# Kernel optimization log

Hardware: AMD Instinct MI355X
Metric: run time of the kernel (lower is better)

The kernel has to match this reference:

```python
import jax, jax.numpy as jnp
import numpy as np

B, S, HID = 8, 1024, 1024
NH, HD = 16, 64  # num heads, head dim
EPS = 1e-12


def setup_inputs() -> dict:
    key = jax.random.key(0)
    ks = jax.random.split(key, 8)
    sc = 0.02
    return {
        "hidden_states": jax.random.normal(ks[0], (B, S, HID), jnp.float32),
        "attention_mask": jnp.zeros((B, 1, 1, S), jnp.bool_),
        "rel_pos": jax.random.normal(ks[1], (1, NH, S, S), jnp.float32),
        "rel_2d_pos": jax.random.normal(ks[2], (1, NH, S, S), jnp.float32),
        "w_qkv": jax.random.normal(ks[3], (3 * HID, HID), jnp.float32) * sc,
        "q_bias": jnp.zeros((1, 1, HID), jnp.float32),
        "v_bias": jnp.zeros((1, 1, HID), jnp.float32),
        "w_out": jax.random.normal(ks[4], (HID, HID), jnp.float32) * sc,
        "b_out": jnp.zeros((HID,), jnp.float32),
        "ln_gamma": jnp.ones((HID,), jnp.float32),
        "ln_beta": jnp.zeros((HID,), jnp.float32),
    }


def reference(hidden_states, attention_mask, rel_pos, rel_2d_pos,
              w_qkv, q_bias, v_bias, w_out, b_out, ln_gamma, ln_beta):
    x = hidden_states
    # fast_qkv: single projection, no bias; then add q_bias/v_bias
    qkv = jnp.einsum('bsh,oh->bso', x, w_qkv)  # [B,S,3*HID]
    q, k, v = jnp.split(qkv, 3, axis=-1)
    q = q + q_bias
    v = v + v_bias
    # [B,S,HID] -> [B,NH,S,HD]
    to_heads = lambda t: t.reshape(B, S, NH, HD).transpose(0, 2, 1, 3)
    qh, kh, vh = to_heads(q), to_heads(k), to_heads(v)
    qh = qh / jnp.sqrt(jnp.float32(HD))
    scores = jnp.einsum('bhqd,bhkd->bhqk', qh, kh)
    scores = scores + rel_pos + rel_2d_pos
    scores = jnp.where(attention_mask, -jnp.inf, scores.astype(jnp.float32))
    probs = jax.nn.softmax(scores, axis=-1).astype(vh.dtype)
    ctx = jnp.einsum('bhqk,bhkd->bhqd', probs, vh)
    ctx = ctx.transpose(0, 2, 1, 3).reshape(B, S, HID)
    # self-output: dense + residual + LayerNorm
    h = jnp.einsum('bsh,oh->bso', ctx, w_out) + b_out + x
    mu = jnp.mean(h, axis=-1, keepdims=True)
    var = jnp.var(h, axis=-1, keepdims=True)
    out = (h - mu) / jnp.sqrt(var + EPS) * ln_gamma + ln_beta
    return out
```

## Files before the change

kernel.cpp:

```cpp
#include <hip/hip_runtime.h>
#include <stdint.h>
#include <stddef.h>

typedef unsigned short u16;
typedef __attribute__((ext_vector_type(8))) short short8;
typedef __attribute__((ext_vector_type(4))) float f32x4;
typedef __attribute__((ext_vector_type(4))) unsigned short ushort4v;
typedef __attribute__((ext_vector_type(4))) unsigned char uchar4v;
typedef __attribute__((ext_vector_type(2))) unsigned int uint2v;

constexpr int B_ = 8, S_ = 1024, HID_ = 1024, NH_ = 16, HD_ = 64;

__device__ __forceinline__ u16 f2b(float f) {
  unsigned int u = __builtin_bit_cast(unsigned int, f);
  u += 0x7fff + ((u >> 16) & 1);
  return (u16)(u >> 16);
}
__device__ __forceinline__ float b2f(u16 s) {
  unsigned int u = ((unsigned int)s) << 16;
  return __builtin_bit_cast(float, u);
}
__device__ __forceinline__ void llds16(const void* g, void* l) {
  __builtin_amdgcn_global_load_lds((__attribute__((address_space(1))) void*)g,
                                   (__attribute__((address_space(3))) void*)l, 16, 0, 0);
}

__global__ __launch_bounds__(256) void prep_cvt(
    const float* __restrict__ x, const float* __restrict__ wqkv,
    const float* __restrict__ wout, u16* __restrict__ xb,
    u16* __restrict__ wqkvb, u16* __restrict__ woutb) {
  const int NX4 = B_ * S_ * HID_ / 4, NW14 = 3 * HID_ * HID_ / 4, NW24 = HID_ * HID_ / 4;
  const int tot = NX4 + NW14 + NW24;
  for (int i = blockIdx.x * blockDim.x + threadIdx.x; i < tot; i += gridDim.x * blockDim.x) {
    const float4* s; u16* d; int j;
    if (i < NX4)              { s = (const float4*)x;    d = xb;    j = i; }
    else if (i < NX4 + NW14)  { s = (const float4*)wqkv; d = wqkvb; j = i - NX4; }
    else                      { s = (const float4*)wout; d = woutb; j = i - NX4 - NW14; }
    float4 v = s[j];
    ushort4v o; o[0] = f2b(v.x); o[1] = f2b(v.y); o[2] = f2b(v.z); o[3] = f2b(v.w);
    *(ushort4v*)(d + 4 * (size_t)j) = o;
  }
}

__global__ __launch_bounds__(256) void rel_perm(
    const float* __restrict__ a, const float* __restrict__ b, u16* __restrict__ relb) {
  __shared__ u16 lbuf[16 * 1032];
  const int qtg = blockIdx.x, h = blockIdx.y;
  const int t = threadIdx.x;
#pragma unroll
  for (int it = 0; it < 16; ++it) {
    int idx = it * 256 + t;
    int lq = idx >> 8, kc = idx & 255;
    size_t src = ((size_t)h * S_ + qtg * 16 + lq) * S_ + kc * 4;
    float4 va = *(const float4*)(a + src);
    float4 vb = *(const float4*)(b + src);
    ushort4v o;
    o[0] = f2b(va.x + vb.x); o[1] = f2b(va.y + vb.y);
    o[2] = f2b(va.z + vb.z); o[3] = f2b(va.w + vb.w);
    *(ushort4v*)(lbuf + lq * 1032 + kc * 4) = o;
  }
  __syncthreads();
#pragma unroll
  for (int it = 0; it < 16; ++it) {
    int c = it * 16 + (t >> 4);
    int ktg = c >> 2, qk = c & 3, lq = t & 15;
    ushort4v v = *(const ushort4v*)(lbuf + lq * 1032 + ktg * 16 + qk * 4);
    *(ushort4v*)(relb + ((((size_t)h * 64 + ktg) * 64 + qtg) * 4 + qk) * 64 + lq * 4) = v;
  }
}

__global__ __launch_bounds__(256) void gemm_qkv(
    const u16* __restrict__ W, const u16* __restrict__ X,
    const float* __restrict__ qbias, const float* __restrict__ vbias,
    u16* __restrict__ Qb, u16* __restrict__ Kb, u16* __restrict__ Vb) {
  constexpr int K = HID_;
  __shared__ u16 smem[128 * 136];
  u16* Ws = smem;
  u16* Xs = smem + 4096;
  const int o0 = blockIdx.x * 128, s0 = blockIdx.y * 128;
  const int t = threadIdx.x, lane = t & 63, wv = t >> 6;
  const int wr = wv >> 1, wc = wv & 1, ln = lane & 15, q8 = lane >> 4;
  f32x4 acc[4][4] = {};

  for (int kt = 0; kt < K / 32; ++kt) {
    const int k0 = kt * 32;
#pragma unroll
    for (int c = 0; c < 2; ++c) {
      int idx = c * 256 + t, row = idx >> 2, cc = (idx & 3) * 8;
      llds16(W + (size_t)(o0 + row) * K + k0 + cc, Ws + (size_t)(c * 256 + wv * 64) * 8);
      llds16(X + (size_t)(s0 + row) * K + k0 + cc, Xs + (size_t)(c * 256 + wv * 64) * 8);
    }
    __syncthreads();
    short8 of[4], sf[4];
#pragma unroll
    for (int mi = 0; mi < 4; ++mi)
      of[mi] = *(const short8*)(Ws + (wr * 64 + mi * 16 + ln) * 32 + q8 * 8);
#pragma unroll
    for (int ni = 0; ni < 4; ++ni)
      sf[ni] = *(const short8*)(Xs + (wc * 64 + ni * 16 + ln) * 32 + q8 * 8);
#pragma unroll
    for (int mi = 0; mi < 4; ++mi)
#pragma unroll
      for (int ni = 0; ni < 4; ++ni)
        acc[mi][ni] = __builtin_amdgcn_mfma_f32_16x16x32_bf16(of[mi], sf[ni], acc[mi][ni], 0, 0, 0);
    __syncthreads();
  }

  const int sec = o0 >> 10;
#pragma unroll
  for (int mi = 0; mi < 4; ++mi) {
    const int ocol = wr * 64 + mi * 16 + q8 * 4;
    const int oo = (o0 + ocol) & 1023;
    float4 b4;
    if (sec == 0)      b4 = *(const float4*)(qbias + oo);
    else if (sec == 2) b4 = *(const float4*)(vbias + oo);
    else               b4 = float4{0.f, 0.f, 0.f, 0.f};
#pragma unroll
    for (int ni = 0; ni < 4; ++ni) {
      const int srow = wc * 64 + ni * 16 + ln;
      u16 e[4];
#pragma unroll
      for (int r = 0; r < 4; ++r) {
        float v = acc[mi][ni][r] + ((const float*)&b4)[r];
        if (sec == 0) v *= 0.125f;
        e[r] = f2b(v);
      }
      uint2v pw;
      pw[0] = (unsigned)e[0] | ((unsigned)e[1] << 16);
      pw[1] = (unsigned)e[2] | ((unsigned)e[3] << 16);
      *(uint2v*)(smem + srow * 136 + ocol) = pw;
    }
  }
  __syncthreads();
  u16* dst = (sec == 0) ? Qb : (sec == 1) ? Kb : Vb;
#pragma unroll
  for (int i = 0; i < 8; ++i) {
    int flat = i * 256 + t;
    int srow = flat >> 4, c8 = (flat & 15) * 8;
    short8 v = *(const short8*)(smem + srow * 136 + c8);
    int oo = (o0 + c8) & 1023, hh = oo >> 6, dd = oo & 63;
    int s = s0 + srow, bb = s >> 10, ss = s & 1023;
    *(short8*)(dst + ((size_t)(bb * NH_ + hh) * S_ + ss) * HD_ + dd) = v;
  }
}

__global__ __launch_bounds__(256) void transpose_v(
    const u16* __restrict__ Vb, u16* __restrict__ Vtb) {
  __shared__ u16 tile[64][72];
  const int st = blockIdx.x * 64, bh = blockIdx.y;
  const int t = threadIdx.x;
#pragma unroll
  for (int i = 0; i < 2; ++i) {
    int idx = i * 256 + t, row = idx >> 3, c8 = (idx & 7) * 8;
    *(short8*)(&tile[row][c8]) = *(const short8*)(Vb + ((size_t)bh * S_ + st + row) * HD_ + c8);
  }
  __syncthreads();
#pragma unroll
  for (int i = 0; i < 2; ++i) {
    int idx = i * 256 + t, d = idx >> 3, c8 = (idx & 7) * 8;
    short8 v;
#pragma unroll
    for (int j = 0; j < 8; ++j) v[j] = (short)tile[c8 + j][d];
    *(short8*)(Vtb + ((size_t)bh * HD_ + d) * S_ + st + c8) = v;
  }
}

__global__ __launch_bounds__(256, 3) void flash_attn(
    const u16* __restrict__ Qb, const u16* __restrict__ Kb,
    const u16* __restrict__ Vtb, const u16* __restrict__ relb,
    const unsigned char* __restrict__ mask, u16* __restrict__ ctxb) {
  const int qt_blk = blockIdx.x, h = blockIdx.y, b = blockIdx.z;
  const int bh = b * NH_ + h, q0 = qt_blk * 128;
  const int t = threadIdx.x, lane = t & 63, wv = t >> 6;
  const int ln = lane & 15, q8 = lane >> 4;

  __shared__ u16 Ks[128 * 72];
  __shared__ u16 Vts[64 * 136];
  __shared__ u16 Pbuf[4 * 32 * 40];
  u16* Pw = Pbuf + wv * 1280;

  const int krow = t >> 3, kcol = (t & 7) * 8;
  const int vrow = t >> 4, vcol = (t & 15) * 8;

  short8 kreg[4], vreg[4];
#pragma unroll
  for (int i = 0; i < 4; ++i)
    kreg[i] = *(const short8*)(Kb + ((size_t)bh * S_ + i * 32 + krow) * HD_ + kcol);
#pragma unroll
  for (int i = 0; i < 4; ++i)
    vreg[i] = *(const short8*)(Vtb + ((size_t)bh * HD_ + i * 16 + vrow) * S_ + vcol);

  short8 qf[2][2];
#pragma unroll
  for (int qt = 0; qt < 2; ++qt)
#pragma unroll
    for (int kc = 0; kc < 2; ++kc)
      qf[qt][kc] = *(const short8*)(Qb + ((size_t)bh * S_ + q0 + wv * 32 + qt * 16 + ln) * HD_ + kc * 32 + q8 * 8);

  f32x4 Oa[4][2] = {};
  float rs2[2] = {0.f, 0.f};

  for (int kt128 = 0; kt128 < 8; ++kt128) {
    const int k0 = kt128 * 128;

    ushort4v relg[4][2][2];
    uchar4v  mg[4][2];
#pragma unroll
    for (int kvc = 0; kvc < 4; ++kvc)
#pragma unroll
      for (int sub = 0; sub < 2; ++sub) {
        const int kt = kvc * 2 + sub, ktg = kt128 * 8 + kt;
        mg[kvc][sub] = *(const uchar4v*)(mask + b * S_ + k0 + kt * 16 + q8 * 4);
#pragma unroll
        for (int qt = 0; qt < 2; ++qt) {
          const int qtg = qt_blk * 8 + wv * 2 + qt;
          relg[kvc][sub][qt] = *(const ushort4v*)(relb +
              ((((size_t)h * 64 + ktg) * 64 + qtg) * 4 + q8) * 64 + ln * 4);
        }
      }

    __syncthreads();
#pragma unroll
    for (int i = 0; i < 4; ++i)
      *(short8*)(Ks + (i * 32 + krow) * 72 + kcol) = kreg[i];
#pragma unroll
    for (int i = 0; i < 4; ++i)
      *(short8*)(Vts + (i * 16 + vrow) * 136 + vcol) = vreg[i];
    if (kt128 < 7) {
      const int k0n = k0 + 128;
#pragma unroll
      for (int i = 0; i < 4; ++i)
        kreg[i] = *(const short8*)(Kb + ((size_t)bh * S_ + k0n + i * 32 + krow) * HD_ + kcol);
#pragma unroll
      for (int i = 0; i < 4; ++i)
        vreg[i] = *(const short8*)(Vtb + ((size_t)bh * HD_ + i * 16 + vrow) * S_ + k0n + vcol);
    }
    __syncthreads();

#pragma unroll
    for (int kvc = 0; kvc < 4; ++kvc) {
#pragma unroll
      for (int sub = 0; sub < 2; ++sub) {
        const int kt = kvc * 2 + sub;
        short8 kf0 = *(const short8*)(Ks + (kt * 16 + ln) * 72 + q8 * 8);
        short8 kf1 = *(const short8*)(Ks + (kt * 16 + ln) * 72 + 32 + q8 * 8);
        uchar4v m4 = mg[kvc][sub];
        f32x4 mbase;
#pragma unroll
        for (int r = 0; r < 4; ++r) mbase[r] = (m4[r] ? -1e30f : 0.f) - 8.0f;
#pragma unroll
        for (int qt = 0; qt < 2; ++qt) {
          ushort4v r4 = relg[kvc][sub][qt];
          f32x4 sc;
#pragma unroll
          for (int r = 0; r < 4; ++r) sc[r] = b2f(r4[r]) + mbase[r];
          sc = __builtin_amdgcn_mfma_f32_16x16x32_bf16(kf0, qf[qt][0], sc, 0, 0, 0);
          sc = __builtin_amdgcn_mfma_f32_16x16x32_bf16(kf1, qf[qt][1], sc, 0, 0, 0);
          float p0 = __expf(sc[0]), p1 = __expf(sc[1]);
          float p2 = __expf(sc[2]), p3 = __expf(sc[3]);
          rs2[qt] += (p0 + p1) + (p2 + p3);
          uint2v pw;
          pw[0] = (unsigned)f2b(p0) | ((unsigned)f2b(p1) << 16);
          pw[1] = (unsigned)f2b(p2) | ((unsigned)f2b(p3) << 16);
          *(uint2v*)(Pw + (qt * 16 + ln) * 40 + sub * 16 + q8 * 4) = pw;
        }
      }
      short8 pf0 = *(const short8*)(Pw + ln * 40 + q8 * 8);
      short8 pf1 = *(const short8*)(Pw + (16 + ln) * 40 + q8 * 8);
#pragma unroll
      for (int mt = 0; mt < 4; ++mt) {
        short8 vf = *(const short8*)(Vts + (mt * 16 + ln) * 136 + kvc * 32 + q8 * 8);
        Oa[mt][0] = __builtin_amdgcn_mfma_f32_16x16x32_bf16(vf, pf0, Oa[mt][0], 0, 0, 0);
        Oa[mt][1] = __builtin_amdgcn_mfma_f32_16x16x32_bf16(vf, pf1, Oa[mt][1], 0, 0, 0);
      }
    }
  }

  float inv[2];
#pragma unroll
  for (int qt = 0; qt < 2; ++qt) {
    rs2[qt] += __shfl_xor(rs2[qt], 16, 64);
    rs2[qt] += __shfl_xor(rs2[qt], 32, 64);
    inv[qt] = 1.f / rs2[qt];
  }

  __syncthreads();
  u16* Ob = Ks + wv * 2304;
#pragma unroll
  for (int qt = 0; qt < 2; ++qt)
#pragma unroll
    for (int mt = 0; mt < 4; ++mt) {
      u16 e[4];
#pragma unroll
      for (int r = 0; r < 4; ++r) e[r] = f2b(Oa[mt][qt][r] * inv[qt]);
      uint2v pw;
      pw[0] = (unsigned)e[0] | ((unsigned)e[1] << 16);
      pw[1] = (unsigned)e[2] | ((unsigned)e[3] << 16);
      *(uint2v*)(Ob + (qt * 16 + ln) * 72 + mt * 16 + q8 * 4) = pw;
    }
#pragma unroll
  for (int p = 0; p < 4; ++p) {
    int row = p * 8 + (lane >> 3);
    int c8 = (lane & 7) * 8;
    short8 v = *(const short8*)(Ob + row * 72 + c8);
    int q = q0 + wv * 32 + row;
    *(short8*)(ctxb + ((size_t)(b * S_ + q)) * HID_ + h * 64 + c8) = v;
  }
}

__global__ __launch_bounds__(256) void gemm_out(
    const u16* __restrict__ W, const u16* __restrict__ X,
    const float* __restrict__ bout, const float* __restrict__ xres,
    u16* __restrict__ hb) {
  constexpr int K = HID_;
  __shared__ u16 smem[128 * 136];
  u16* Ws = smem;
  u16* Xs = smem + 4096;
  const int o0 = blockIdx.x * 128, s0 = blockIdx.y * 128;
  const int t = threadIdx.x, lane = t & 63, wv = t >> 6;
  const int wr = wv >> 1, wc = wv & 1, ln = lane & 15, q8 = lane >> 4;
  f32x4 acc[4][4] = {};

  for (int kt = 0; kt < K / 32; ++kt) {
    const int k0 = kt * 32;
#pragma unroll
    for (int c = 0; c < 2; ++c) {
      int idx = c * 256 + t, row = idx >> 2, cc = (idx & 3) * 8;
      llds16(W + (size_t)(o0 + row) * K + k0 + cc, Ws + (size_t)(c * 256 + wv * 64) * 8);
      llds16(X + (size_t)(s0 + row) * K + k0 + cc, Xs + (size_t)(c * 256 + wv * 64) * 8);
    }
    __syncthreads();
    short8 of[4], sf[4];
#pragma unroll
    for (int mi = 0; mi < 4; ++mi)
      of[mi] = *(const short8*)(Ws + (wr * 64 + mi * 16 + ln) * 32 + q8 * 8);
#pragma unroll
    for (int ni = 0; ni < 4; ++ni)
      sf[ni] = *(const short8*)(Xs + (wc * 64 + ni * 16 + ln) * 32 + q8 * 8);
#pragma unroll
    for (int mi = 0; mi < 4; ++mi)
#pragma unroll
      for (int ni = 0; ni < 4; ++ni)
        acc[mi][ni] = __builtin_amdgcn_mfma_f32_16x16x32_bf16(of[mi], sf[ni], acc[mi][ni], 0, 0, 0);
    __syncthreads();
  }

#pragma unroll
  for (int mi = 0; mi < 4; ++mi) {
    const int ocol = wr * 64 + mi * 16 + q8 * 4;
    float4 b4 = *(const float4*)(bout + o0 + ocol);
#pragma unroll
    for (int ni = 0; ni < 4; ++ni) {
      const int srow = wc * 64 + ni * 16 + ln;
      u16 e[4];
#pragma unroll
      for (int r = 0; r < 4; ++r) e[r] = f2b(acc[mi][ni][r] + ((const float*)&b4)[r]);
      uint2v pw;
      pw[0] = (unsigned)e[0] | ((unsigned)e[1] << 16);
      pw[1] = (unsigned)e[2] | ((unsigned)e[3] << 16);
      *(uint2v*)(smem + srow * 136 + ocol) = pw;
    }
  }
  __syncthreads();
#pragma unroll
  for (int i = 0; i < 8; ++i) {
    int flat = i * 256 + t;
    int srow = flat >> 4, c8 = (flat & 15) * 8;
    short8 v = *(const short8*)(smem + srow * 136 + c8);
    int s = s0 + srow, o = o0 + c8;
    float4 x0 = *(const float4*)(xres + (size_t)s * HID_ + o);
    float4 x1 = *(const float4*)(xres + (size_t)s * HID_ + o + 4);
    short8 st;
#pragma unroll
    for (int j = 0; j < 4; ++j) st[j] = (short)f2b(b2f((u16)v[j]) + ((const float*)&x0)[j]);
#pragma unroll
    for (int j = 0; j < 4; ++j) st[4 + j] = (short)f2b(b2f((u16)v[4 + j]) + ((const float*)&x1)[j]);
    *(short8*)(hb + (size_t)s * HID_ + o) = st;
  }
}

__global__ __launch_bounds__(256) void ln_kernel(
    const u16* __restrict__ hb, const float* __restrict__ gamma,
    const float* __restrict__ beta, float* __restrict__ out) {
  const int lane = threadIdx.x & 63, wv = threadIdx.x >> 6;
  const int row = blockIdx.x * 4 + wv;
  const u16* hr = hb + (size_t)row * HID_;
  float v[16];
  short8 a = *(const short8*)(hr + lane * 16);
  short8 c = *(const short8*)(hr + lane * 16 + 8);
#pragma unroll
  for (int j = 0; j < 8; ++j) { v[j] = b2f((u16)a[j]); v[8 + j] = b2f((u16)c[j]); }
  float sum = 0.f, sq = 0.f;
#pragma unroll
  for (int j = 0; j < 16; ++j) { sum += v[j]; sq += v[j] * v[j]; }
#pragma unroll
  for (int off = 1; off < 64; off <<= 1) {
    sum += __shfl_xor(sum, off, 64);
    sq  += __shfl_xor(sq, off, 64);
  }
  const float mu = sum * (1.f / HID_);
  const float var = sq * (1.f / HID_) - mu * mu;
  const float inv = 1.f / sqrtf(var + 1e-12f);
#pragma unroll
  for (int j = 0; j < 16; ++j) {
    const int n = lane * 16 + j;
    out[(size_t)row * HID_ + n] = (v[j] - mu) * inv * gamma[n] + beta[n];
  }
}

extern "C" void kernel_launch(void* const* d_in, const int* in_sizes, int n_in,
                              void* d_out, int out_size, void* d_ws, size_t ws_size,
                              hipStream_t stream) {
  (void)in_sizes; (void)n_in; (void)out_size; (void)ws_size;
  const float* x     = (const float*)d_in[0];
  const unsigned char* mask = (const unsigned char*)d_in[1];
  const float* relp  = (const float*)d_in[2];
  const float* rel2  = (const float*)d_in[3];
  const float* wqkv  = (const float*)d_in[4];
  const float* qbias = (const float*)d_in[5];
  const float* vbias = (const float*)d_in[6];
  const float* wout  = (const float*)d_in[7];
  const float* bout  = (const float*)d_in[8];
  const float* gamma = (const float*)d_in[9];
  const float* beta  = (const float*)d_in[10];
  float* out = (float*)d_out;

  char* ws = (char*)d_ws;
  const size_t MB = (size_t)1 << 20;
  u16* xb    = (u16*)(ws + 0 * MB);
  u16* wqkvb = (u16*)(ws + 16 * MB);
  u16* woutb = (u16*)(ws + 22 * MB);
  u16* relb  = (u16*)(ws + 24 * MB);
  u16* Qb    = (u16*)(ws + 56 * MB);
  u16* Kb    = (u16*)(ws + 72 * MB);
  u16* Vb    = (u16*)(ws + 88 * MB);
  u16* ctxb  = (u16*)(ws + 104 * MB);
  u16* hb    = (u16*)(ws + 120 * MB);
  u16* Vtb   = xb;

  prep_cvt<<<1024, 256, 0, stream>>>(x, wqkv, wout, xb, wqkvb, woutb);
  rel_perm<<<dim3(64, 16), 256, 0, stream>>>(relp, rel2, relb);
  gemm_qkv<<<dim3(24, 64), 256, 0, stream>>>(wqkvb, xb, qbias, vbias, Qb, Kb, Vb);
  transpose_v<<<dim3(16, 128), 256, 0, stream>>>(Vb, Vtb);
  flash_attn<<<dim3(8, 16, 8), 256, 0, stream>>>(Qb, Kb, Vtb, relb, mask, ctxb);
  gemm_out<<<dim3(8, 64), 256, 0, stream>>>(woutb, ctxb, bout, x, hb);
  ln_kernel<<<2048, 256, 0, stream>>>(hb, gamma, beta, out);
}
```

Measured before the change: 444.7 us.

## Fuse V transpose into QKV GEMM epilogue, use exp2 softmax, remap attention grid

The QKV GEMM now writes V straight into the transposed [bh, d, s] layout through shared memory, which removes the separate transpose_v kernel and its round trip through global memory. The softmax is moved to base 2: log2(e) is folded into the Q scale and into the precomputed relative-position bias so exp2f can replace __expf. The flash-attention grid becomes a 1D launch with a swizzled block-to-(head, q-tile, batch) mapping, meant to place blocks that share the same head's relative-bias tiles close in time for better L2 reuse. The V epilogue writes shared memory with scalar, strided stores that may cause bank conflicts, and the bf16 rounding of the bias now happens after scaling.

```diff
diff --git a/kernel.cpp b/kernel.cpp
--- a/kernel.cpp
+++ b/kernel.cpp
@@ -10,6 +10,9 @@
 typedef __attribute__((ext_vector_type(2))) unsigned int uint2v;
 
 constexpr int B_ = 8, S_ = 1024, HID_ = 1024, NH_ = 16, HD_ = 64;
+#define LOG2E_F 1.4426950408889634f
+#define QSCALE_F 0.18033688011112043f
+#define SHIFT2_F 11.541560327111707f
 
 __device__ __forceinline__ u16 f2b(float f) {
   unsigned int u = __builtin_bit_cast(unsigned int, f);
@@ -55,8 +58,8 @@
     float4 va = *(const float4*)(a + src);
     float4 vb = *(const float4*)(b + src);
     ushort4v o;
-    o[0] = f2b(va.x + vb.x); o[1] = f2b(va.y + vb.y);
-    o[2] = f2b(va.z + vb.z); o[3] = f2b(va.w + vb.w);
+    o[0] = f2b((va.x + vb.x) * LOG2E_F); o[1] = f2b((va.y + vb.y) * LOG2E_F);
+    o[2] = f2b((va.z + vb.z) * LOG2E_F); o[3] = f2b((va.w + vb.w) * LOG2E_F);
     *(ushort4v*)(lbuf + lq * 1032 + kc * 4) = o;
   }
   __syncthreads();
@@ -72,7 +75,7 @@
 __global__ __launch_bounds__(256) void gemm_qkv(
     const u16* __restrict__ W, const u16* __restrict__ X,
     const float* __restrict__ qbias, const float* __restrict__ vbias,
-    u16* __restrict__ Qb, u16* __restrict__ Kb, u16* __restrict__ Vb) {
+    u16* __restrict__ Qb, u16* __restrict__ Kb, u16* __restrict__ Vtb) {
   constexpr int K = HID_;
   __shared__ u16 smem[128 * 136];
   u16* Ws = smem;
@@ -107,14 +110,41 @@
   }
 
   const int sec = o0 >> 10;
+
+  if (sec == 2) {
+#pragma unroll
+    for (int mi = 0; mi < 4; ++mi) {
+      const int ocol = wr * 64 + mi * 16 + q8 * 4;
+      const int oo = (o0 + ocol) & 1023;
+      float4 b4 = *(const float4*)(vbias + oo);
+#pragma unroll
+      for (int ni = 0; ni < 4; ++ni) {
+        const int srow = wc * 64 + ni * 16 + ln;
+#pragma unroll
+        for (int r = 0; r < 4; ++r)
+          smem[(ocol + r) * 136 + srow] = f2b(acc[mi][ni][r] + ((const float*)&b4)[r]);
+      }
+    }
+    __syncthreads();
+#pragma unroll
+    for (int i = 0; i < 8; ++i) {
+      int flat = i * 256 + t;
+      int dl = flat >> 4, s8 = (flat & 15) * 8;
+      short8 v = *(const short8*)(smem + dl * 136 + s8);
+      int oo = (o0 + dl) & 1023, hh = oo >> 6, dd = oo & 63;
+      int bb = s0 >> 10, ss = (s0 + s8) & 1023;
+      *(short8*)(Vtb + ((size_t)(bb * NH_ + hh) * HD_ + dd) * S_ + ss) = v;
+    }
+    return;
+  }
+
 #pragma unroll
   for (int mi = 0; mi < 4; ++mi) {
     const int ocol = wr * 64 + mi * 16 + q8 * 4;
     const int oo = (o0 + ocol) & 1023;
     float4 b4;
-    if (sec == 0)      b4 = *(const float4*)(qbias + oo);
-    else if (sec == 2) b4 = *(const float4*)(vbias + oo);
-    else               b4 = float4{0.f, 0.f, 0.f, 0.f};
+    if (sec == 0) b4 = *(const float4*)(qbias + oo);
+    else          b4 = float4{0.f, 0.f, 0.f, 0.f};
 #pragma unroll
     for (int ni = 0; ni < 4; ++ni) {
       const int srow = wc * 64 + ni * 16 + ln;
@@ -122,7 +152,7 @@
 #pragma unroll
       for (int r = 0; r < 4; ++r) {
         float v = acc[mi][ni][r] + ((const float*)&b4)[r];
-        if (sec == 0) v *= 0.125f;
+        if (sec == 0) v *= QSCALE_F;
         e[r] = f2b(v);
       }
       uint2v pw;
@@ -132,7 +162,7 @@
     }
   }
   __syncthreads();
-  u16* dst = (sec == 0) ? Qb : (sec == 1) ? Kb : Vb;
+  u16* dst = (sec == 0) ? Qb : Kb;
 #pragma unroll
   for (int i = 0; i < 8; ++i) {
     int flat = i * 256 + t;
@@ -144,32 +174,13 @@
   }
 }
 
-__global__ __launch_bounds__(256) void transpose_v(
-    const u16* __restrict__ Vb, u16* __restrict__ Vtb) {
-  __shared__ u16 tile[64][72];
-  const int st = blockIdx.x * 64, bh = blockIdx.y;
-  const int t = threadIdx.x;
-#pragma unroll
-  for (int i = 0; i < 2; ++i) {
-    int idx = i * 256 + t, row = idx >> 3, c8 = (idx & 7) * 8;
-    *(short8*)(&tile[row][c8]) = *(const short8*)(Vb + ((size_t)bh * S_ + st + row) * HD_ + c8);
-  }
-  __syncthreads();
-#pragma unroll
-  for (int i = 0; i < 2; ++i) {
-    int idx = i * 256 + t, d = idx >> 3, c8 = (idx & 7) * 8;
-    short8 v;
-#pragma unroll
-    for (int j = 0; j < 8; ++j) v[j] = (short)tile[c8 + j][d];
-    *(short8*)(Vtb + ((size_t)bh * HD_ + d) * S_ + st + c8) = v;
-  }
-}
-
 __global__ __launch_bounds__(256, 3) void flash_attn(
     const u16* __restrict__ Qb, const u16* __restrict__ Kb,
     const u16* __restrict__ Vtb, const u16* __restrict__ relb,
     const unsigned char* __restrict__ mask, u16* __restrict__ ctxb) {
-  const int qt_blk = blockIdx.x, h = blockIdx.y, b = blockIdx.z;
+  const int lin = blockIdx.x;
+  const int virt = (lin & 7) * 128 + (lin >> 3);
+  const int h = virt >> 6, qt_blk = (virt >> 3) & 7, b = virt & 7;
   const int bh = b * NH_ + h, q0 = qt_blk * 128;
   const int t = threadIdx.x, lane = t & 63, wv = t >> 6;
   const int ln = lane & 15, q8 = lane >> 4;
@@ -247,7 +258,7 @@
         uchar4v m4 = mg[kvc][sub];
         f32x4 mbase;
 #pragma unroll
-        for (int r = 0; r < 4; ++r) mbase[r] = (m4[r] ? -1e30f : 0.f) - 8.0f;
+        for (int r = 0; r < 4; ++r) mbase[r] = (m4[r] ? -1e30f : 0.f) - SHIFT2_F;
 #pragma unroll
         for (int qt = 0; qt < 2; ++qt) {
           ushort4v r4 = relg[kvc][sub][qt];
@@ -256,8 +267,8 @@
           for (int r = 0; r < 4; ++r) sc[r] = b2f(r4[r]) + mbase[r];
           sc = __builtin_amdgcn_mfma_f32_16x16x32_bf16(kf0, qf[qt][0], sc, 0, 0, 0);
           sc = __builtin_amdgcn_mfma_f32_16x16x32_bf16(kf1, qf[qt][1], sc, 0, 0, 0);
-          float p0 = __expf(sc[0]), p1 = __expf(sc[1]);
-          float p2 = __expf(sc[2]), p3 = __expf(sc[3]);
+          float p0 = exp2f(sc[0]), p1 = exp2f(sc[1]);
+          float p2 = exp2f(sc[2]), p3 = exp2f(sc[3]);
           rs2[qt] += (p0 + p1) + (p2 + p3);
           uint2v pw;
           pw[0] = (unsigned)f2b(p0) | ((unsigned)f2b(p1) << 16);
@@ -433,16 +444,14 @@
   u16* relb  = (u16*)(ws + 24 * MB);
   u16* Qb    = (u16*)(ws + 56 * MB);
   u16* Kb    = (u16*)(ws + 72 * MB);
-  u16* Vb    = (u16*)(ws + 88 * MB);
+  u16* Vtb   = (u16*)(ws + 88 * MB);
   u16* ctxb  = (u16*)(ws + 104 * MB);
   u16* hb    = (u16*)(ws + 120 * MB);
-  u16* Vtb   = xb;
 
   prep_cvt<<<1024, 256, 0, stream>>>(x, wqkv, wout, xb, wqkvb, woutb);
   rel_perm<<<dim3(64, 16), 256, 0, stream>>>(relp, rel2, relb);
-  gemm_qkv<<<dim3(24, 64), 256, 0, stream>>>(wqkvb, xb, qbias, vbias, Qb, Kb, Vb);
-  transpose_v<<<dim3(16, 128), 256, 0, stream>>>(Vb, Vtb);
-  flash_attn<<<dim3(8, 16, 8), 256, 0, stream>>>(Qb, Kb, Vtb, relb, mask, ctxb);
+  gemm_qkv<<<dim3(24, 64), 256, 0, stream>>>(wqkvb, xb, qbias, vbias, Qb, Kb, Vtb);
+  flash_attn<<<1024, 256, 0, stream>>>(Qb, Kb, Vtb, relb, mask, ctxb);
   gemm_out<<<dim3(8, 64), 256, 0, stream>>>(woutb, ctxb, bout, x, hb);
   ln_kernel<<<2048, 256, 0, stream>>>(hb, gamma, beta, out);
 }
```

Measured after the change: 444.7 us. No clear change (-0.0%).
